# Kernel optimization log

Hardware: AMD Instinct MI355X
Metric: run time of the kernel (lower is better)

The kernel has to match this reference:

```python
import jax, jax.numpy as jnp
import numpy as np

EMBED_DIM = 1024
NUM_HEADS = 16
HEAD_DIM = EMBED_DIM // NUM_HEADS
B, T = 8, 1024


def setup_inputs() -> dict:
    key = jax.random.key(0)
    ks = jax.random.split(key, 8)
    s = EMBED_DIM ** -0.5
    return {
        "query": jax.random.normal(ks[0], (B, T, EMBED_DIM), jnp.float32),
        "key": jax.random.normal(ks[1], (B, T, EMBED_DIM), jnp.float32),
        "value": jax.random.normal(ks[2], (B, T, EMBED_DIM), jnp.float32),
        "key_padding_mask": jnp.zeros((B, T), dtype=bool),
        "attn_mask": jax.random.normal(ks[3], (T, T), jnp.float32) * 0.02,
        "in_proj_weight": jax.random.normal(ks[4], (3 * EMBED_DIM, EMBED_DIM), jnp.float32) * s,
        "in_proj_bias": jax.random.normal(ks[5], (3 * EMBED_DIM,), jnp.float32) * 0.02,
        "out_proj_weight": jax.random.normal(ks[6], (EMBED_DIM, EMBED_DIM), jnp.float32) * s,
        "out_proj_bias": jax.random.normal(ks[7], (EMBED_DIM,), jnp.float32) * 0.02,
    }


def reference(query, key, value, key_padding_mask, attn_mask,
              in_proj_weight, in_proj_bias, out_proj_weight, out_proj_bias):
    E, H, Dh = EMBED_DIM, NUM_HEADS, HEAD_DIM
    scale = Dh ** -0.5
    w_q, w_k, w_v = in_proj_weight[:E], in_proj_weight[E:2 * E], in_proj_weight[2 * E:]
    b_q, b_k, b_v = in_proj_bias[:E], in_proj_bias[E:2 * E], in_proj_bias[2 * E:]

    b, t_q, _ = query.shape
    t_k = key.shape[1]
    # projections: F.linear(x, W, b) = x @ W.T + b
    q = (query @ w_q.T + b_q).reshape(b, t_q, H, Dh).transpose(0, 2, 1, 3)
    k = (key @ w_k.T + b_k).reshape(b, t_k, H, Dh).transpose(0, 2, 1, 3)
    v = (value @ w_v.T + b_v).reshape(b, t_k, H, Dh).transpose(0, 2, 1, 3)

    scores = jnp.einsum('bhqd,bhkd->bhqk', q, k) * scale  # [B,H,Tq,Tk]
    scores = jnp.where(key_padding_mask[:, None, None, :], -jnp.inf, scores)
    scores = scores + attn_mask  # broadcast [Tq,Tk] over batch/heads
    attn = jax.nn.softmax(scores, axis=-1)
    out = jnp.einsum('bhqk,bhkd->bhqd', attn, v)
    out = out.transpose(0, 2, 1, 3).reshape(b, t_q, E)
    return out @ out_proj_weight.T + out_proj_bias
```

## Files before the change

### kernel.cpp

```cpp
#include <hip/hip_runtime.h>
#include <cstdint>
#include <cstddef>

#define E_DIM   1024
#define NHEADS  16
#define DHEAD   64
#define BATCH   8
#define SEQ     1024
#define MROWS   (BATCH*SEQ)

#define LOG2E 1.44269504f

typedef __bf16 bf16;
typedef __attribute__((ext_vector_type(8))) __bf16 bf16x8;
typedef __attribute__((ext_vector_type(4))) __bf16 bf16x4;
typedef __attribute__((ext_vector_type(4))) float f32x4;

typedef const __attribute__((address_space(1))) unsigned int gu32;
typedef __attribute__((address_space(3))) unsigned int lu32;

__global__ __launch_bounds__(256)
void split_kernel(const float* __restrict__ src, bf16* __restrict__ hi,
                  bf16* __restrict__ lo, int n4)
{
    int i = blockIdx.x * 256 + threadIdx.x;
    if (i >= n4) return;
    float4 x = ((const float4*)src)[i];
    bf16x4 h, l;
    h[0] = (bf16)x.x; l[0] = (bf16)(x.x - (float)h[0]);
    h[1] = (bf16)x.y; l[1] = (bf16)(x.y - (float)h[1]);
    h[2] = (bf16)x.z; l[2] = (bf16)(x.z - (float)h[2]);
    h[3] = (bf16)x.w; l[3] = (bf16)(x.w - (float)h[3]);
    ((bf16x4*)hi)[i] = h;
    ((bf16x4*)lo)[i] = l;
}

__global__ __launch_bounds__(256)
void cvt_bf16_kernel(const float* __restrict__ src, bf16* __restrict__ dst,
                     float scale, int n4)
{
    int i = blockIdx.x * 256 + threadIdx.x;
    if (i >= n4) return;
    float4 x = ((const float4*)src)[i];
    bf16x4 h;
    h[0] = (bf16)(x.x * scale); h[1] = (bf16)(x.y * scale);
    h[2] = (bf16)(x.z * scale); h[3] = (bf16)(x.w * scale);
    ((bf16x4*)dst)[i] = h;
}

template<int AMODE>
__global__ __launch_bounds__(512, 2)
void gemm_nt_mfma(const float* __restrict__ Af,
                  const bf16* __restrict__ Ahi, const bf16* __restrict__ Alo,
                  const bf16* __restrict__ Whi, const bf16* __restrict__ Wlo,
                  const float* __restrict__ bias,
                  float* __restrict__ outF, bf16* __restrict__ outHi,
                  int M, int N, int K, int mode)
{
    __shared__ char  smemA[2][16384];
    __shared__ bf16  Whs[2][128 * 32];
    __shared__ bf16  Wls[2][128 * 32];

    const int tid  = threadIdx.x;
    const int lane = tid & 63;
    const int wid  = tid >> 6;
    const int wm = (wid >> 1) * 32;
    const int wn = (wid & 1) * 64;
    const int fr = lane & 15;
    const int fq = lane >> 4;
    const int fk = ((fq + (fr >> 1)) & 3) * 8;

    const int mBase = blockIdx.y * 128;
    const int nBase = blockIdx.x * 128;

    const int rowW  = tid >> 2;
    const int colW  = (((tid & 3) - ((tid >> 3) & 3)) & 3) * 8;
    const int rowAf  = tid >> 3;
    const int slotAf = ((tid & 7) - (rowAf & 7)) & 7;

    const int dcol = lane & 15;
    float bv[4];
#pragma unroll
    for (int bn = 0; bn < 4; ++bn)
        bv[bn] = bias[nBase + wn + bn * 16 + dcol];

    f32x4 acc[2][4];
#pragma unroll
    for (int i = 0; i < 2; ++i)
#pragma unroll
        for (int j = 0; j < 4; ++j) acc[i][j] = (f32x4){0.f, 0.f, 0.f, 0.f};

    const float* pAf0 = Af  + (size_t)(mBase + rowAf) * K + slotAf * 4;
    const float* pAf1 = pAf0 + (size_t)64 * K;
    const bf16*  pAh  = Ahi + (size_t)(mBase + rowW) * K + colW;
    const bf16*  pAl  = Alo + (size_t)(mBase + rowW) * K + colW;
    const bf16*  pWh  = Whi + (size_t)(nBase + rowW) * K + colW;
    const bf16*  pWl  = Wlo + (size_t)(nBase + rowW) * K + colW;

    auto stage = [&](int bi) {
        if (AMODE == 1) {
            float* As = (float*)smemA[bi];
            __builtin_amdgcn_global_load_lds((gu32*)pAf0, (lu32*)&As[wid * 256],        16, 0, 0);
            __builtin_amdgcn_global_load_lds((gu32*)pAf1, (lu32*)&As[2048 + wid * 256], 16, 0, 0);
            pAf0 += 32; pAf1 += 32;
        } else {
            bf16* Ah = (bf16*)smemA[bi];
            bf16* Al = Ah + 4096;
            __builtin_amdgcn_global_load_lds((gu32*)pAh, (lu32*)&Ah[wid * 512], 16, 0, 0);
            __builtin_amdgcn_global_load_lds((gu32*)pAl, (lu32*)&Al[wid * 512], 16, 0, 0);
            pAh += 32; pAl += 32;
        }
        __builtin_amdgcn_global_load_lds((gu32*)pWh, (lu32*)&Whs[bi][wid * 512], 16, 0, 0);
        __builtin_amdgcn_global_load_lds((gu32*)pWl, (lu32*)&Wls[bi][wid * 512], 16, 0, 0);
        pWh += 32; pWl += 32;
    };

    stage(0);

    const int NIT = K >> 5;
#pragma unroll 1
    for (int it = 0; it < NIT; ++it) {
        const int cur = it & 1;
        if (it + 1 < NIT) {
            stage(cur ^ 1);
            asm volatile("s_waitcnt vmcnt(4)" ::: "memory");
        } else {
            asm volatile("s_waitcnt vmcnt(0)" ::: "memory");
        }
        __builtin_amdgcn_s_barrier();

        bf16x8 afh[2], afl[2], bfh[4], bfl[4];
        if (AMODE == 1) {
            const float* As = (const float*)smemA[cur];
#pragma unroll
            for (int am = 0; am < 2; ++am) {
                const int row = wm + am * 16 + fr;
                const float* Ar = &As[row * 32];
                f32x4 a0 = *(const f32x4*)&Ar[((2 * fq     + (fr & 7)) & 7) * 4];
                f32x4 a1 = *(const f32x4*)&Ar[((2 * fq + 1 + (fr & 7)) & 7) * 4];
                bf16x8 h, l;
#pragma unroll
                for (int j = 0; j < 4; ++j) {
                    h[j]     = (bf16)a0[j];
                    l[j]     = (bf16)(a0[j] - (float)h[j]);
                    h[j + 4] = (bf16)a1[j];
                    l[j + 4] = (bf16)(a1[j] - (float)h[j + 4]);
                }
                afh[am] = h; afl[am] = l;
            }
        } else {
            const bf16* Ah = (const bf16*)smemA[cur];
            const bf16* Al = Ah + 4096;
#pragma unroll
            for (int am = 0; am < 2; ++am) {
                afh[am] = *(const bf16x8*)&Ah[(wm + am * 16 + fr) * 32 + fk];
                afl[am] = *(const bf16x8*)&Al[(wm + am * 16 + fr) * 32 + fk];
            }
        }
#pragma unroll
        for (int bn = 0; bn < 4; ++bn) {
            bfh[bn] = *(const bf16x8*)&Whs[cur][(wn + bn * 16 + fr) * 32 + fk];
            bfl[bn] = *(const bf16x8*)&Wls[cur][(wn + bn * 16 + fr) * 32 + fk];
        }
        __builtin_amdgcn_s_setprio(1);
#pragma unroll
        for (int am = 0; am < 2; ++am)
#pragma unroll
            for (int bn = 0; bn < 4; ++bn) {
                acc[am][bn] = __builtin_amdgcn_mfma_f32_16x16x32_bf16(afh[am], bfh[bn], acc[am][bn], 0, 0, 0);
                acc[am][bn] = __builtin_amdgcn_mfma_f32_16x16x32_bf16(afh[am], bfl[bn], acc[am][bn], 0, 0, 0);
                acc[am][bn] = __builtin_amdgcn_mfma_f32_16x16x32_bf16(afl[am], bfh[bn], acc[am][bn], 0, 0, 0);
            }
        __builtin_amdgcn_s_setprio(0);
        __builtin_amdgcn_s_barrier();
    }

    const int drow = (lane >> 4) * 4;
#pragma unroll
    for (int bn = 0; bn < 4; ++bn) {
        const int col = nBase + wn + bn * 16 + dcol;
#pragma unroll
        for (int am = 0; am < 2; ++am) {
#pragma unroll
            for (int r = 0; r < 4; ++r) {
                const int row = mBase + wm + am * 16 + drow + r;
                const float v = acc[am][bn][r] + bv[bn];
                if (mode == 0) {
                    outF[(size_t)row * N + col] = v;
                } else {
                    const int b = row >> 10, t = row & 1023;
                    const int h = col >> 6,  d = col & 63;
                    size_t idx;
                    if (mode == 1)
                        idx = (((size_t)(b * NHEADS + h)) * SEQ + t) * DHEAD + d;
                    else
                        idx = (((size_t)(b * NHEADS + h)) * DHEAD + d) * SEQ + t;
                    outHi[idx] = (bf16)v;
                }
            }
        }
    }
}

__global__ __launch_bounds__(512)
void attn_mfma_kernel(const bf16* __restrict__ qkv,
                      const bf16* __restrict__ mask_bf,
                      const unsigned char* __restrict__ kpad,
                      bf16* __restrict__ ctx_hi, bf16* __restrict__ ctx_lo)
{
    __shared__ bf16 Ks [2][4096];
    __shared__ bf16 Vts[2][4096];
    __shared__ bf16 Pn[8][1024];

    const int tid  = threadIdx.x;
    const int lane = tid & 63;
    const int wid  = tid >> 6;
    const int c16  = lane & 15;
    const int quad = lane >> 4;

    const int bh = blockIdx.x;
    const int qt = blockIdx.y;
    const int b = bh >> 4, h = bh & 15;

    const size_t seg = (size_t)MROWS * E_DIM;
    const size_t headoff = (size_t)bh * SEQ * DHEAD;
    const bf16* Q_g  = qkv + headoff;
    const bf16* K_g  = qkv + seg + headoff;
    const bf16* Vt_g = qkv + 2 * seg + headoff;

    const int qglob = qt * 128 + wid * 16 + c16;

    bf16x8 qf[2];
#pragma unroll
    for (int ks = 0; ks < 2; ++ks)
        qf[ks] = *(const bf16x8*)&Q_g[(size_t)qglob * DHEAD + quad * 8 + ks * 32];

    float l_i = 0.f;
    f32x4 oacc[4];
#pragma unroll
    for (int dt = 0; dt < 4; ++dt) oacc[dt] = (f32x4){0.f, 0.f, 0.f, 0.f};

    const int row0 = tid >> 3;
    const int c0   = (tid & 7) ^ (row0 & 7);

    auto stage = [&](int kt, int bi) {
        const int ktb = kt * 64;
        const size_t k0 = (size_t)(ktb + row0) * DHEAD + c0 * 8;
        const size_t v0 = (size_t)row0 * SEQ + ktb + c0 * 8;
        __builtin_amdgcn_global_load_lds((gu32*)(K_g + k0),  (lu32*)&Ks [bi][wid * 512], 16, 0, 0);
        __builtin_amdgcn_global_load_lds((gu32*)(Vt_g + v0), (lu32*)&Vts[bi][wid * 512], 16, 0, 0);
    };

    stage(0, 0);
    __syncthreads();

    const int pxor = (c16 & 7) << 3;
    const size_t kpb = (size_t)b * SEQ + quad * 4;

#pragma unroll 1
    for (int kt = 0; kt < 16; ++kt) {
        const int cur = kt & 1;
        const int ktb = kt * 64;

        bf16x4 mvh[4];
        unsigned kpu[4];
#pragma unroll
        for (int st = 0; st < 4; ++st) {
            mvh[st] = *(const bf16x4*)&mask_bf[(size_t)qglob * SEQ + ktb + st * 16 + quad * 4];
            kpu[st] = *(const unsigned*)&kpad[kpb + ktb + st * 16];
        }

        if (kt < 15) stage(kt + 1, cur ^ 1);

        f32x4 sacc[4];
#pragma unroll
        for (int st = 0; st < 4; ++st) sacc[st] = (f32x4){0.f, 0.f, 0.f, 0.f};
        __builtin_amdgcn_s_setprio(1);
#pragma unroll
        for (int st = 0; st < 4; ++st) {
            const int row = st * 16 + c16;
            const int sw  = row & 7;
#pragma unroll
            for (int ks = 0; ks < 2; ++ks) {
                const int cp = ((quad + ks * 4) ^ sw);
                bf16x8 kh = *(const bf16x8*)&Ks[cur][(row * 8 + cp) * 8];
                sacc[st] = __builtin_amdgcn_mfma_f32_16x16x32_bf16(kh, qf[ks], sacc[st], 0, 0, 0);
            }
        }
        __builtin_amdgcn_s_setprio(0);

        float s[16];
#pragma unroll
        for (int st = 0; st < 4; ++st) {
#pragma unroll
            for (int r = 0; r < 4; ++r)
                s[st * 4 + r] = fmaf(sacc[st][r], 0.125f * LOG2E, (float)mvh[st][r]);
        }
        if (__any((kpu[0] | kpu[1] | kpu[2] | kpu[3]) != 0u)) {
#pragma unroll
            for (int st = 0; st < 4; ++st)
#pragma unroll
                for (int r = 0; r < 4; ++r)
                    if ((kpu[st] >> (r * 8)) & 0xff) s[st * 4 + r] = -2e30f;
        }
        float p[16];
#pragma unroll
        for (int i = 0; i < 16; ++i)
            p[i] = __builtin_amdgcn_exp2f(fminf(s[i], 30.f));
        float u8[8];
#pragma unroll
        for (int i = 0; i < 8; ++i) u8[i] = p[i] + p[i + 8];
#pragma unroll
        for (int i = 0; i < 4; ++i) u8[i] += u8[i + 4];
        float ps = (u8[0] + u8[1]) + (u8[2] + u8[3]);
        ps += __shfl_xor(ps, 16, 64);
        ps += __shfl_xor(ps, 32, 64);
        l_i += ps;

#pragma unroll
        for (int st = 0; st < 4; ++st) {
            bf16x4 ph;
#pragma unroll
            for (int r = 0; r < 4; ++r) ph[r] = (bf16)p[st * 4 + r];
            *(bf16x4*)&Pn[wid][c16 * 64 + ((st * 16 + quad * 4) ^ pxor)] = ph;
        }
        bf16x8 pf[2];
#pragma unroll
        for (int ks = 0; ks < 2; ++ks)
            pf[ks] = *(const bf16x8*)&Pn[wid][c16 * 64 + ((ks * 32 + quad * 8) ^ pxor)];

        __builtin_amdgcn_s_setprio(1);
#pragma unroll
        for (int dt = 0; dt < 4; ++dt) {
            const int row = dt * 16 + c16;
            const int sw  = row & 7;
#pragma unroll
            for (int ks = 0; ks < 2; ++ks) {
                const int cp = ((quad + ks * 4) ^ sw);
                bf16x8 vh = *(const bf16x8*)&Vts[cur][(row * 8 + cp) * 8];
                oacc[dt] = __builtin_amdgcn_mfma_f32_16x16x32_bf16(vh, pf[ks], oacc[dt], 0, 0, 0);
            }
        }
        __builtin_amdgcn_s_setprio(0);

        __syncthreads();
    }

    const float invl = 1.0f / l_i;
#pragma unroll
    for (int dt = 0; dt < 4; ++dt) {
        bf16x4 oh, ol;
#pragma unroll
        for (int r = 0; r < 4; ++r) {
            float v = oacc[dt][r] * invl;
            oh[r] = (bf16)v;
            ol[r] = (bf16)(v - (float)oh[r]);
        }
        size_t idx = ((size_t)b * SEQ + qglob) * E_DIM + h * DHEAD + dt * 16 + quad * 4;
        *(bf16x4*)&ctx_hi[idx] = oh;
        *(bf16x4*)&ctx_lo[idx] = ol;
    }
}

extern "C" void kernel_launch(void* const* d_in, const int* in_sizes, int n_in,
                              void* d_out, int out_size, void* d_ws, size_t ws_size,
                              hipStream_t stream)
{
    const float* inputs[3] = { (const float*)d_in[0], (const float*)d_in[1],
                               (const float*)d_in[2] };
    const unsigned char* kpad = (const unsigned char*)d_in[3];
    const float* attn_mask = (const float*)d_in[4];
    const float* w_in  = (const float*)d_in[5];
    const float* b_in  = (const float*)d_in[6];
    const float* w_out = (const float*)d_in[7];
    const float* b_out = (const float*)d_in[8];
    float* out = (float*)d_out;

    char* ws = (char*)d_ws;
    const size_t MB = 1024 * 1024;
    bf16* w_in_hi  = (bf16*)(ws + 0 * MB);
    bf16* w_in_lo  = (bf16*)(ws + 6 * MB);
    bf16* w_out_hi = (bf16*)(ws + 12 * MB);
    bf16* w_out_lo = (bf16*)(ws + 14 * MB);
    bf16* qkv      = (bf16*)(ws + 16 * MB);
    bf16* mask_bf  = (bf16*)(ws + 64 * MB);
    bf16* ctx_hi   = (bf16*)(ws + 66 * MB);
    bf16* ctx_lo   = (bf16*)(ws + 82 * MB);

    const size_t seg = (size_t)MROWS * E_DIM;

    split_kernel<<<(3 * E_DIM * E_DIM / 4 + 255) / 256, 256, 0, stream>>>(
        w_in, w_in_hi, w_in_lo, 3 * E_DIM * E_DIM / 4);
    split_kernel<<<(E_DIM * E_DIM / 4 + 255) / 256, 256, 0, stream>>>(
        w_out, w_out_hi, w_out_lo, E_DIM * E_DIM / 4);
    cvt_bf16_kernel<<<(SEQ * SEQ / 4 + 255) / 256, 256, 0, stream>>>(
        attn_mask, mask_bf, LOG2E, SEQ * SEQ / 4);

    for (int z = 0; z < 3; ++z) {
        gemm_nt_mfma<1><<<dim3(E_DIM / 128, MROWS / 128), 512, 0, stream>>>(
            inputs[z], nullptr, nullptr,
            w_in_hi + (size_t)z * E_DIM * E_DIM, w_in_lo + (size_t)z * E_DIM * E_DIM,
            b_in + z * E_DIM,
            nullptr, qkv + (size_t)z * seg,
            MROWS, E_DIM, E_DIM, (z == 2) ? 2 : 1);
    }

    attn_mfma_kernel<<<dim3(BATCH * NHEADS, SEQ / 128), 512, 0, stream>>>(
        qkv, mask_bf, kpad, ctx_hi, ctx_lo);

    gemm_nt_mfma<0><<<dim3(E_DIM / 128, MROWS / 128), 512, 0, stream>>>(
        nullptr, ctx_hi, ctx_lo, w_out_hi, w_out_lo, b_out,
        out, nullptr, MROWS, E_DIM, E_DIM, 0);
}
```

Before: 466.0 us.

## Merge QKV projections into one launch and swizzle tile order for L2 reuse

The three separate input-projection GEMM launches become one launch with blockIdx.y selecting Q, K or V, and each block's tile index is remapped so groups of 8 M-tiles by 8 N-tiles run together. This removes launch gaps and tail underutilisation between the three GEMMs, and improves L2/MALL reuse of A rows and weight columns. It adds per-block pointer selection and a small amount of index arithmetic.

```diff
diff --git a/kernel.cpp b/kernel.cpp
--- a/kernel.cpp
+++ b/kernel.cpp
@@ -50,12 +50,13 @@
 
 template<int AMODE>
 __global__ __launch_bounds__(512, 2)
-void gemm_nt_mfma(const float* __restrict__ Af,
+void gemm_nt_mfma(const float* __restrict__ Af0, const float* __restrict__ Af1,
+                  const float* __restrict__ Af2,
                   const bf16* __restrict__ Ahi, const bf16* __restrict__ Alo,
                   const bf16* __restrict__ Whi, const bf16* __restrict__ Wlo,
                   const float* __restrict__ bias,
                   float* __restrict__ outF, bf16* __restrict__ outHi,
-                  int M, int N, int K, int mode)
+                  int M, int N, int K)
 {
     __shared__ char  smemA[2][16384];
     __shared__ bf16  Whs[2][128 * 32];
@@ -70,8 +71,18 @@
     const int fq = lane >> 4;
     const int fk = ((fq + (fr >> 1)) & 3) * 8;
 
-    const int mBase = blockIdx.y * 128;
-    const int nBase = blockIdx.x * 128;
+    const int z = blockIdx.y;
+    const float* Af = (z == 0) ? Af0 : (z == 1) ? Af1 : Af2;
+    const bf16* Wh = Whi + (size_t)z * E_DIM * E_DIM;
+    const bf16* Wl = Wlo + (size_t)z * E_DIM * E_DIM;
+    const float* bs = bias + z * E_DIM;
+    const int mode = AMODE ? ((z == 2) ? 2 : 1) : 0;
+
+    const int id = blockIdx.x;
+    const int mTile = (id & 7) + 8 * (id >> 6);
+    const int nTile = (id >> 3) & 7;
+    const int mBase = mTile * 128;
+    const int nBase = nTile * 128;
 
     const int rowW  = tid >> 2;
     const int colW  = (((tid & 3) - ((tid >> 3) & 3)) & 3) * 8;
@@ -82,7 +93,7 @@
     float bv[4];
 #pragma unroll
     for (int bn = 0; bn < 4; ++bn)
-        bv[bn] = bias[nBase + wn + bn * 16 + dcol];
+        bv[bn] = bs[nBase + wn + bn * 16 + dcol];
 
     f32x4 acc[2][4];
 #pragma unroll
@@ -94,8 +105,8 @@
     const float* pAf1 = pAf0 + (size_t)64 * K;
     const bf16*  pAh  = Ahi + (size_t)(mBase + rowW) * K + colW;
     const bf16*  pAl  = Alo + (size_t)(mBase + rowW) * K + colW;
-    const bf16*  pWh  = Whi + (size_t)(nBase + rowW) * K + colW;
-    const bf16*  pWl  = Wlo + (size_t)(nBase + rowW) * K + colW;
+    const bf16*  pWh  = Wh + (size_t)(nBase + rowW) * K + colW;
+    const bf16*  pWl  = Wl + (size_t)(nBase + rowW) * K + colW;
 
     auto stage = [&](int bi) {
         if (AMODE == 1) {
@@ -108,11 +119,10 @@
             bf16* Al = Ah + 4096;
             __builtin_amdgcn_global_load_lds((gu32*)pAh, (lu32*)&Ah[wid * 512], 16, 0, 0);
             __builtin_amdgcn_global_load_lds((gu32*)pAl, (lu32*)&Al[wid * 512], 16, 0, 0);
-            pAh += 32; pAl += 32;
         }
         __builtin_amdgcn_global_load_lds((gu32*)pWh, (lu32*)&Whs[bi][wid * 512], 16, 0, 0);
         __builtin_amdgcn_global_load_lds((gu32*)pWl, (lu32*)&Wls[bi][wid * 512], 16, 0, 0);
-        pWh += 32; pWl += 32;
+        pAh += 32; pAl += 32; pWh += 32; pWl += 32;
     };
 
     stage(0);
@@ -195,7 +205,7 @@
                         idx = (((size_t)(b * NHEADS + h)) * SEQ + t) * DHEAD + d;
                     else
                         idx = (((size_t)(b * NHEADS + h)) * DHEAD + d) * SEQ + t;
-                    outHi[idx] = (bf16)v;
+                    outHi[(size_t)z * MROWS * E_DIM + idx] = (bf16)v;
                 }
             }
         }
@@ -366,8 +376,9 @@
                               void* d_out, int out_size, void* d_ws, size_t ws_size,
                               hipStream_t stream)
 {
-    const float* inputs[3] = { (const float*)d_in[0], (const float*)d_in[1],
-                               (const float*)d_in[2] };
+    const float* q_in = (const float*)d_in[0];
+    const float* k_in = (const float*)d_in[1];
+    const float* v_in = (const float*)d_in[2];
     const unsigned char* kpad = (const unsigned char*)d_in[3];
     const float* attn_mask = (const float*)d_in[4];
     const float* w_in  = (const float*)d_in[5];
@@ -387,8 +398,6 @@
     bf16* ctx_hi   = (bf16*)(ws + 66 * MB);
     bf16* ctx_lo   = (bf16*)(ws + 82 * MB);
 
-    const size_t seg = (size_t)MROWS * E_DIM;
-
     split_kernel<<<(3 * E_DIM * E_DIM / 4 + 255) / 256, 256, 0, stream>>>(
         w_in, w_in_hi, w_in_lo, 3 * E_DIM * E_DIM / 4);
     split_kernel<<<(E_DIM * E_DIM / 4 + 255) / 256, 256, 0, stream>>>(
@@ -396,19 +405,19 @@
     cvt_bf16_kernel<<<(SEQ * SEQ / 4 + 255) / 256, 256, 0, stream>>>(
         attn_mask, mask_bf, LOG2E, SEQ * SEQ / 4);
 
-    for (int z = 0; z < 3; ++z) {
-        gemm_nt_mfma<1><<<dim3(E_DIM / 128, MROWS / 128), 512, 0, stream>>>(
-            inputs[z], nullptr, nullptr,
-            w_in_hi + (size_t)z * E_DIM * E_DIM, w_in_lo + (size_t)z * E_DIM * E_DIM,
-            b_in + z * E_DIM,
-            nullptr, qkv + (size_t)z * seg,
-            MROWS, E_DIM, E_DIM, (z == 2) ? 2 : 1);
-    }
+    gemm_nt_mfma<1><<<dim3(512, 3), 512, 0, stream>>>(
+        q_in, k_in, v_in,
+        nullptr, nullptr,
+        w_in_hi, w_in_lo, b_in,
+        nullptr, qkv,
+        MROWS, E_DIM, E_DIM);
 
     attn_mfma_kernel<<<dim3(BATCH * NHEADS, SEQ / 128), 512, 0, stream>>>(
         qkv, mask_bf, kpad, ctx_hi, ctx_lo);
 
-    gemm_nt_mfma<0><<<dim3(E_DIM / 128, MROWS / 128), 512, 0, stream>>>(
-        nullptr, ctx_hi, ctx_lo, w_out_hi, w_out_lo, b_out,
-        out, nullptr, MROWS, E_DIM, E_DIM, 0);
+    gemm_nt_mfma<0><<<dim3(512, 1), 512, 0, stream>>>(
+        nullptr, nullptr, nullptr,
+        ctx_hi, ctx_lo, w_out_hi, w_out_lo, b_out,
+        out, nullptr,
+        MROWS, E_DIM, E_DIM);
 }
```

After: 446.5 us. -4.2%, faster.
